# Kernel optimization log

Hardware: AMD Instinct MI355X
Metric: run time of the kernel (lower is better)

## Reference

```python
import jax, jax.numpy as jnp
import numpy as np

N = 16384        # nodes
E = 262144       # edges (avg degree 16)
MUL = 64         # multiplicity per irrep
RDIM = 8         # radial embedding dim
NEURONS = 64     # radial MLP hidden width
NSPECIES = 4
AVG_NEIGH = 16.0
SQRT3 = 1.7320508075688772


def setup_inputs() -> dict:
    key = jax.random.key(0)
    k = jax.random.split(key, 16)
    ey1 = jax.random.normal(k[3], (E, 3), jnp.float32)
    ey1 = ey1 / jnp.linalg.norm(ey1, axis=-1, keepdims=True)  # l=1 spherical harmonics ~ unit edge vectors
    return {
        'node_x0': jax.random.normal(k[0], (N, MUL), jnp.float32),
        'node_x1': jax.random.normal(k[1], (N, MUL, 3), jnp.float32),
        'edge_y0': jnp.ones((E,), jnp.float32),            # l=0 SH is constant
        'edge_y1': ey1,
        'radial_embedding': jax.random.uniform(k[4], (E, RDIM), jnp.float32),
        'senders': jax.random.randint(k[5], (E,), 0, N, dtype=jnp.int32),
        'receivers': jax.random.randint(k[6], (E,), 0, N, dtype=jnp.int32),
        'node_species': jax.random.randint(k[7], (N,), 0, NSPECIES, dtype=jnp.int32),
        'Wup0': jax.random.normal(k[8], (MUL, MUL), jnp.float32),
        'Wup1': jax.random.normal(k[9], (MUL, MUL), jnp.float32),
        'Rw1': jax.random.normal(k[10], (RDIM, NEURONS), jnp.float32),
        'Rw2': jax.random.normal(k[11], (NEURONS, 4 * MUL), jnp.float32),
        'Wd0': jax.random.normal(k[12], (2 * MUL, 2 * MUL), jnp.float32),
        'Wd1': jax.random.normal(k[13], (2 * MUL, MUL), jnp.float32),
        'Wsc0': jax.random.normal(k[14], (NSPECIES, MUL, 2 * MUL), jnp.float32),
        'Wsc1': jax.random.normal(k[15], (NSPECIES, MUL, MUL), jnp.float32),
    }


def reference(node_x0, node_x1, edge_y0, edge_y1, radial_embedding,
              senders, receivers, node_species,
              Wup0, Wup1, Rw1, Rw2, Wd0, Wd1, Wsc0, Wsc1):
    inv = 1.0 / jnp.sqrt(jnp.float32(MUL))
    # ---- linear_up: per-irrep channel mixing --------------------------------
    h0 = (node_x0 @ Wup0) * inv                              # [N, MUL] 0e
    h1 = jnp.einsum('nmc,mk->nkc', node_x1, Wup1) * inv      # [N, MUL, 3] 1o
    # ---- radial MLP -> per-edge tensor-product path weights -----------------
    hid = jax.nn.silu((radial_embedding @ Rw1) / jnp.sqrt(jnp.float32(RDIM)))
    w = ((hid @ Rw2) / jnp.sqrt(jnp.float32(NEURONS))).reshape(E, 4, MUL)
    # ---- gather sender features ---------------------------------------------
    s0 = h0[senders]                                         # [E, MUL]
    s1 = h1[senders]                                         # [E, MUL, 3]
    # ---- CG tensor product (lmax=1) with radial weights ----------------------
    m0a = w[:, 0] * s0 * edge_y0[:, None]                    # 0e x 0e -> 0e
    m0b = w[:, 1] * jnp.einsum('emc,ec->em', s1, edge_y1) / SQRT3  # 1o . 1o -> 0e
    m1a = w[:, 2][:, :, None] * s0[:, :, None] * edge_y1[:, None, :]  # 0e x 1o -> 1o
    m1b = w[:, 3][:, :, None] * s1 * edge_y0[:, None, None]          # 1o x 0e -> 1o
    # ---- scatter-sum to receivers, normalize by sqrt(avg_num_neighbours) ----
    denom = jnp.sqrt(jnp.float32(AVG_NEIGH))
    a0 = jax.ops.segment_sum(jnp.concatenate([m0a, m0b], axis=-1), receivers, num_segments=N) / denom  # [N, 2*MUL]
    a1 = jax.ops.segment_sum(jnp.concatenate([m1a, m1b], axis=1), receivers, num_segments=N) / denom   # [N, 2*MUL, 3]
    # ---- linear_down to gate irreps (MUL scalars + MUL gates, MUL vectors) ---
    inv2 = 1.0 / jnp.sqrt(jnp.float32(2 * MUL))
    d0 = (a0 @ Wd0) * inv2                                   # [N, 2*MUL]
    d1 = jnp.einsum('nmc,mk->nkc', a1, Wd1) * inv2           # [N, MUL, 3]
    # ---- species-indexed self connection (gather weights by species) --------
    all0 = jnp.einsum('nm,smk->nsk', node_x0, Wsc0) * inv    # [N, S, 2*MUL]
    sc0 = jnp.take_along_axis(all0, node_species[:, None, None], axis=1)[:, 0]
    all1 = jnp.einsum('nmc,smk->nskc', node_x1, Wsc1) * inv  # [N, S, MUL, 3]
    sc1 = jnp.take_along_axis(all1, node_species[:, None, None, None], axis=1)[:, 0]
    f0 = 0.5 * (d0 + sc0)
    f1 = 0.5 * (d1 + sc1)
    # ---- equivariant gate: even_act on scalars, even_gate_act on gates ------
    scalars = jax.nn.silu(f0[:, :MUL])                       # [N, MUL]
    gates = jax.nn.silu(f0[:, MUL:])                         # [N, MUL]
    vectors = f1 * gates[:, :, None]                         # [N, MUL, 3]
    return scalars, vectors
```

## Files before the change

### kernel.cpp

```cpp
#include <hip/hip_runtime.h>

#define NN 16384
#define NE 262144
#define N64 (NN * 64)

typedef unsigned short u16;
typedef __attribute__((ext_vector_type(8))) short short8;
typedef __attribute__((ext_vector_type(4))) float f32x4;

__device__ __forceinline__ float us2f(u16 u) {
    union { unsigned int i; float f; } v; v.i = ((unsigned int)u) << 16; return v.f;
}
__device__ __forceinline__ u16 f2us(float x) {
    union { float f; unsigned int i; } u; u.f = x;
    unsigned int r = u.i + 0x7FFF + ((u.i >> 16) & 1);
    return (u16)(r >> 16);
}
__device__ __forceinline__ float silu_f(float x) { return x / (1.0f + __expf(-x)); }
__device__ __forceinline__ float ldf(const void* p, long i, int f) {
    return f ? ((const float*)p)[i] : us2f(((const u16*)p)[i]);
}
__device__ __forceinline__ void ld8(const void* p, long v8, int f, float* o) {
    if (f) {
        const f32x4* q = (const f32x4*)p + v8 * 2;
        f32x4 a = q[0], b = q[1];
        o[0] = a[0]; o[1] = a[1]; o[2] = a[2]; o[3] = a[3];
        o[4] = b[0]; o[5] = b[1]; o[6] = b[2]; o[7] = b[3];
    } else {
        short8 s = ((const short8*)p)[v8];
#pragma unroll
        for (int j = 0; j < 8; j++) o[j] = us2f((u16)s[j]);
    }
}
__device__ __forceinline__ void st8(u16* d, const float* o) {
    short8 s;
#pragma unroll
    for (int j = 0; j < 8; j++) s[j] = (short)f2us(o[j]);
    *reinterpret_cast<short8*>(d) = s;
}
__device__ __forceinline__ short8 f32x8_to_bf16(const float* p) {
    f32x4 a = *reinterpret_cast<const f32x4*>(p);
    f32x4 b = *reinterpret_cast<const f32x4*>(p + 4);
    short8 r;
    r[0] = (short)f2us(a[0]); r[1] = (short)f2us(a[1]);
    r[2] = (short)f2us(a[2]); r[3] = (short)f2us(a[3]);
    r[4] = (short)f2us(b[0]); r[5] = (short)f2us(b[1]);
    r[6] = (short)f2us(b[2]); r[7] = (short)f2us(b[3]);
    return r;
}

__global__ void k_sniff(const u16* __restrict__ re, int* __restrict__ flag) {
    int t = threadIdx.x;
    int hit = (re[t] >= 0x4000) ? 1 : 0;
    unsigned long long b = __ballot(hit);
    if (t == 0) *flag = (__popcll(b) >= 4) ? 1 : 0;
}

#define SB0 1048576L
#define SB1 4194304L
#define SB2 4456448L
#define SB3 5242880L
#define SB4 7340032L
#define SB5 7344128L
#define SB6 7348224L
#define SB7 7348736L
#define SB8 7365120L
#define SB9 7381504L
#define SB10 7389696L
#define SB11 7422464L
#define SB12 7438848L

__global__ void k_convert(const void* x0, const void* x1, const void* ey0, const void* ey1,
                          const void* re, const void* Wup0, const void* Wup1, const void* Rw1,
                          const void* Rw2, const void* Wd0, const void* Wd1, const void* Wsc0,
                          const void* Wsc1, const int* __restrict__ flag,
                          const int* __restrict__ recv, int* __restrict__ cnt,
                          u16* c_x0, u16* x1T, u16* c_ey0, u16* c_ey1, u16* c_re,
                          u16* c_Wup0, u16* c_Wup1, u16* c_Rw1, u16* c_Rw2,
                          u16* c_Wd0, u16* c_Wd1, u16* c_Wsc0, u16* c_Wsc1) {
    long i = (long)blockIdx.x * 256 + threadIdx.x;
    int f = *flag;
    if (i < NE) atomicAdd(&cnt[recv[i]], 1);
    if (i < 131072) {
        float o[8]; ld8(x0, i, f, o); st8(c_x0 + i * 8, o);
    } else if (i < 262144) {
        long v = i - 131072;
        int n = (int)(v >> 3), k8 = (int)(v & 7);
        long b8 = (long)n * 24 + (long)k8 * 3;
        float o[24];
        ld8(x1, b8, f, o); ld8(x1, b8 + 1, f, o + 8); ld8(x1, b8 + 2, f, o + 16);
#pragma unroll
        for (int c = 0; c < 3; c++) {
            float t[8];
#pragma unroll
            for (int k = 0; k < 8; k++) t[k] = o[k * 3 + c];
            st8(x1T + (long)c * N64 + (long)n * 64 + k8 * 8, t);
        }
    } else if (i < 294912) {
        long v = i - 262144; float o[8]; ld8(ey0, v, f, o); st8(c_ey0 + v * 8, o);
    } else if (i < 393216) {
        long v = i - 294912; float o[8]; ld8(ey1, v, f, o); st8(c_ey1 + v * 8, o);
    } else if (i < 655360) {
        long v = i - 393216; float o[8]; ld8(re, v, f, o); st8(c_re + v * 8, o);
    } else {
        long t = i - 655360;
        if (t < 4096)       { long r = t >> 6, c = t & 63;
                              c_Wup0[c * 64 + r] = f2us(ldf(Wup0, t, f)); }
        else if (t < 8192)  { t -= 4096; long r = t >> 6, c = t & 63;
                              c_Wup1[c * 64 + r] = f2us(ldf(Wup1, t, f)); }
        else if (t < 8704)  { t -= 8192; c_Rw1[t] = f2us(ldf(Rw1, t, f)); }
        else if (t < 25088) { t -= 8704; long r = t >> 8, c = t & 255;
                              c_Rw2[c * 64 + r] = f2us(ldf(Rw2, t, f)); }
        else if (t < 41472) { t -= 25088; long r = t >> 7, c = t & 127;
                              c_Wd0[c * 128 + r] = f2us(ldf(Wd0, t, f)); }
        else if (t < 49664) { t -= 41472; long r = t >> 6, c = t & 63;
                              c_Wd1[c * 128 + r] = f2us(ldf(Wd1, t, f)); }
        else if (t < 82432) { t -= 49664; long s = t >> 13, rm = t & 8191;
                              long r = rm >> 7, c = rm & 127;
                              c_Wsc0[s * 8192 + c * 64 + r] = f2us(ldf(Wsc0, t, f)); }
        else                { t -= 82432; long s = t >> 12, rm = t & 4095;
                              long r = rm >> 6, c = rm & 63;
                              c_Wsc1[s * 4096 + c * 64 + r] = f2us(ldf(Wsc1, t, f)); }
    }
}

__global__ void k_scan(const int* __restrict__ cnt, int* __restrict__ offs,
                       int* __restrict__ cursor) {
    __shared__ int sd[256];
    int t = threadIdx.x;
    int base = t * 64;
    const int4* c4 = (const int4*)cnt;
    int loc[64];
#pragma unroll
    for (int i = 0; i < 16; i++) {
        int4 v = c4[t * 16 + i];
        loc[i * 4 + 0] = v.x; loc[i * 4 + 1] = v.y; loc[i * 4 + 2] = v.z; loc[i * 4 + 3] = v.w;
    }
    int sum = 0;
#pragma unroll
    for (int i = 0; i < 64; i++) sum += loc[i];
    sd[t] = sum; __syncthreads();
    for (int off = 1; off < 256; off <<= 1) {
        int v = (t >= off) ? sd[t - off] : 0;
        __syncthreads();
        sd[t] += v;
        __syncthreads();
    }
    int run = sd[t] - sum;
    for (int i = 0; i < 64; i++) {
        offs[base + i] = run; cursor[base + i] = run;
        run += loc[i];
    }
    if (t == 255) offs[NN] = run;
}

__global__ void k_scatter(const int* __restrict__ recv, const int* __restrict__ senders,
                          const u16* __restrict__ ey0, const u16* __restrict__ ey1,
                          int* __restrict__ cursor, int4* __restrict__ meta) {
    int e = blockIdx.x * 256 + threadIdx.x;
    int node = recv[e];
    int p = atomicAdd(&cursor[node], 1);
    unsigned y0  = ey0[e];
    unsigned y1x = ey1[(long)e * 3 + 0];
    unsigned y1y = ey1[(long)e * 3 + 1];
    unsigned y1z = ey1[(long)e * 3 + 2];
    int4 m;
    m.x = senders[e];
    m.y = (int)(y0 | (y1x << 16));
    m.z = (int)(y1y | (y1z << 16));
    m.w = (int)((unsigned)e | ((unsigned)node << 18));
    meta[p] = m;
}

__global__ void k_up_gemm(const u16* __restrict__ x0, const u16* __restrict__ x1T,
                          const u16* __restrict__ Wup0, const u16* __restrict__ Wup1,
                          u16* __restrict__ h) {
    int inst = blockIdx.y;
    int wv = threadIdx.x >> 6, lane = threadIdx.x & 63;
    int lhi = lane >> 4, llo = lane & 15;
    int mb = blockIdx.x * 256 + wv * 64;
    const u16* B = (inst == 0) ? Wup0 : Wup1;
    const u16* A = (inst == 0) ? x0 : (x1T + (long)(inst - 1) * N64);

    short8 bfr[4][2];
#pragma unroll
    for (int t = 0; t < 4; t++)
#pragma unroll
        for (int s = 0; s < 2; s++)
            bfr[t][s] = *reinterpret_cast<const short8*>(B + (long)(t * 16 + llo) * 64 + s * 32 + lhi * 8);

    f32x4 acc[4][4];
#pragma unroll
    for (int i = 0; i < 4; i++)
#pragma unroll
        for (int t = 0; t < 4; t++) acc[i][t] = 0.0f;

#pragma unroll
    for (int s = 0; s < 2; s++) {
        short8 af[4];
#pragma unroll
        for (int i = 0; i < 4; i++)
            af[i] = *reinterpret_cast<const short8*>(A + (long)(mb + i * 16 + llo) * 64 + s * 32 + lhi * 8);
#pragma unroll
        for (int i = 0; i < 4; i++)
#pragma unroll
            for (int t = 0; t < 4; t++)
                acc[i][t] = __builtin_amdgcn_mfma_f32_16x16x32_bf16(af[i], bfr[t][s], acc[i][t], 0, 0, 0);
    }
#pragma unroll
    for (int i = 0; i < 4; i++)
#pragma unroll
        for (int t = 0; t < 4; t++)
#pragma unroll
            for (int r = 0; r < 4; r++)
                h[(long)(mb + i * 16 + lhi * 4 + r) * 256 + (t * 16 + llo) * 4 + inst] =
                    f2us(acc[i][t][r] * 0.125f);
}

#define RROW 268
__global__ void __launch_bounds__(256, 4)
k_edge(const u16* __restrict__ re, const u16* __restrict__ Rw1,
       const u16* __restrict__ Rw2, const int4* __restrict__ meta,
       const u16* __restrict__ h, float* __restrict__ abuf32) {
    __shared__ u16 w_lds[64 * RROW];
    u16 (*hid_s)[72] = reinterpret_cast<u16 (*)[72]>(w_lds);

    int tid = threadIdx.x;
    int wv = tid >> 6, lane = tid & 63, lhi = lane >> 4, llo = lane & 15;
    int p0 = blockIdx.x * 64;

    {
        int el = tid >> 2;
        int jb = (tid & 3) * 16;
        int e = ((const int*)meta)[(long)(p0 + el) * 4 + 3] & 0x3FFFF;
        short8 r8 = *reinterpret_cast<const short8*>(re + (long)e * 8);
        float rr[8];
#pragma unroll
        for (int r = 0; r < 8; r++) rr[r] = us2f((u16)r8[r]);
        float hv[16];
#pragma unroll
        for (int q = 0; q < 2; q++) {
            short8 w8 = *reinterpret_cast<const short8*>(Rw1 + jb + q * 8);
#pragma unroll
            for (int j = 0; j < 8; j++) hv[q * 8 + j] = rr[0] * us2f((u16)w8[j]);
        }
#pragma unroll
        for (int r = 1; r < 8; r++) {
#pragma unroll
            for (int q = 0; q < 2; q++) {
                short8 w8 = *reinterpret_cast<const short8*>(Rw1 + (long)r * 64 + jb + q * 8);
#pragma unroll
                for (int j = 0; j < 8; j++) hv[q * 8 + j] += rr[r] * us2f((u16)w8[j]);
            }
        }
#pragma unroll
        for (int q = 0; q < 4; q++) {
            ushort4 pk;
            pk.x = f2us(silu_f(hv[q * 4 + 0] * 0.35355339059327373f));
            pk.y = f2us(silu_f(hv[q * 4 + 1] * 0.35355339059327373f));
            pk.z = f2us(silu_f(hv[q * 4 + 2] * 0.35355339059327373f));
            pk.w = f2us(silu_f(hv[q * 4 + 3] * 0.35355339059327373f));
            *reinterpret_cast<ushort4*>(&hid_s[el][jb + q * 4]) = pk;
        }
    }
    __syncthreads();

    {
        short8 bfr[4][2];
#pragma unroll
        for (int t = 0; t < 4; t++)
#pragma unroll
            for (int s = 0; s < 2; s++)
                bfr[t][s] = *reinterpret_cast<const short8*>(
                    Rw2 + (long)(wv * 64 + t * 16 + llo) * 64 + s * 32 + lhi * 8);
        f32x4 acc[4][4];
#pragma unroll
        for (int i = 0; i < 4; i++)
#pragma unroll
            for (int t = 0; t < 4; t++) acc[i][t] = 0.0f;
#pragma unroll
        for (int s = 0; s < 2; s++) {
            short8 af[4];
#pragma unroll
            for (int i = 0; i < 4; i++)
                af[i] = *reinterpret_cast<const short8*>(&hid_s[i * 16 + llo][s * 32 + lhi * 8]);
#pragma unroll
            for (int i = 0; i < 4; i++)
#pragma unroll
                for (int t = 0; t < 4; t++)
                    acc[i][t] = __builtin_amdgcn_mfma_f32_16x16x32_bf16(af[i], bfr[t][s], acc[i][t], 0, 0, 0);
        }
        __syncthreads();
#pragma unroll
        for (int i = 0; i < 4; i++)
#pragma unroll
            for (int t = 0; t < 4; t++)
#pragma unroll
                for (int r = 0; r < 4; r++)
                    w_lds[(i * 16 + lhi * 4 + r) * RROW + wv * 64 + t * 16 + llo] =
                        f2us(acc[i][t][r] * 0.125f);
    }
    __syncthreads();

    {
        const float qn = 0.25f;
        const float rs3 = 0.57735026918962576f;
        int l = lane;
        int base = wv * 16;
        float acc[8];
#pragma unroll
        for (int r = 0; r < 8; r++) acc[r] = 0.f;
        int cur = -1;

        int4 ma = meta[p0 + base];
        ushort4 ha = *reinterpret_cast<const ushort4*>(h + (long)ma.x * 256 + l * 4);
        int4 mb_ = meta[p0 + base + 1];
        ushort4 hb = *reinterpret_cast<const ushort4*>(h + (long)mb_.x * 256 + l * 4);

        for (int ss = 0; ss < 16; ss++) {
            int4 mc = mb_; ushort4 hc = hb;
            if (ss + 2 < 16) {
                mc = meta[p0 + base + ss + 2];
                hc = *reinterpret_cast<const ushort4*>(h + (long)mc.x * 256 + l * 4);
            }
            int node = (int)(((unsigned)ma.w) >> 18);
            if (node != cur) {
                if (cur >= 0) {
                    float* dst = abuf32 + (long)cur * 512 + l;
                    atomicAdd(dst,        acc[0] * qn);
                    atomicAdd(dst + 64,   acc[1] * qn * rs3);
                    atomicAdd(dst + 128,  acc[2] * qn);
                    atomicAdd(dst + 192,  acc[3] * qn);
                    atomicAdd(dst + 256,  acc[4] * qn);
                    atomicAdd(dst + 320,  acc[5] * qn);
                    atomicAdd(dst + 384,  acc[6] * qn);
                    atomicAdd(dst + 448,  acc[7] * qn);
                }
                cur = node;
#pragma unroll
                for (int r = 0; r < 8; r++) acc[r] = 0.f;
            }
            int sl = base + ss;
            float w0 = us2f(w_lds[sl * RROW + l]);
            float w1 = us2f(w_lds[sl * RROW + 64 + l]);
            float w2 = us2f(w_lds[sl * RROW + 128 + l]);
            float w3 = us2f(w_lds[sl * RROW + 192 + l]);
            float y0  = us2f((u16)((unsigned)ma.y & 0xffff));
            float y1x = us2f((u16)((unsigned)ma.y >> 16));
            float y1y = us2f((u16)((unsigned)ma.z & 0xffff));
            float y1z = us2f((u16)((unsigned)ma.z >> 16));
            float s0 = us2f(ha.x), s1x = us2f(ha.y), s1y = us2f(ha.z), s1z = us2f(ha.w);
            acc[0] += w0 * s0 * y0;
            acc[1] += w1 * (s1x * y1x + s1y * y1y + s1z * y1z);
            acc[2] += w2 * s0 * y1x;  acc[3] += w3 * s1x * y0;
            acc[4] += w2 * s0 * y1y;  acc[5] += w3 * s1y * y0;
            acc[6] += w2 * s0 * y1z;  acc[7] += w3 * s1z * y0;
            ma = mb_; ha = hb; mb_ = mc; hb = hc;
        }
        {
            float* dst = abuf32 + (long)cur * 512 + l;
            atomicAdd(dst,        acc[0] * qn);
            atomicAdd(dst + 64,   acc[1] * qn * rs3);
            atomicAdd(dst + 128,  acc[2] * qn);
            atomicAdd(dst + 192,  acc[3] * qn);
            atomicAdd(dst + 256,  acc[4] * qn);
            atomicAdd(dst + 320,  acc[5] * qn);
            atomicAdd(dst + 384,  acc[6] * qn);
            atomicAdd(dst + 448,  acc[7] * qn);
        }
    }
}

#define DN 32
__global__ void __launch_bounds__(320, 3)
k_down(const float* __restrict__ abuf32, const u16* __restrict__ x0,
       const u16* __restrict__ x1T, const int* __restrict__ species,
       const u16* __restrict__ Wd0T, const u16* __restrict__ Wd1T,
       const u16* __restrict__ Wsc0T, const u16* __restrict__ Wsc1T,
       float* __restrict__ out) {
    __shared__ float gate_s[DN][65];
    __shared__ float vec_s[DN * 192];
    __shared__ int sp_s[DN];
    int tid = threadIdx.x;
    int g = tid >> 6;
    int lane = tid & 63, lhi = lane >> 4, llo = lane & 15;
    int node0 = blockIdx.x * DN;
    if (tid < DN) sp_s[tid] = species[node0 + tid];
    __syncthreads();

    const float* Ad; const u16* BdT; int bcol;
    const u16* As; const u16* BsT; int sstr;
    if (g <= 1) { Ad = abuf32; BdT = Wd0T; bcol = g * 64; As = x0; BsT = Wsc0T; sstr = 8192; }
    else        { Ad = abuf32 + (g - 1) * 128; BdT = Wd1T; bcol = 0;
                  As = x1T + (long)(g - 2) * N64; BsT = Wsc1T; sstr = 4096; }

    const float inv2 = 0.08838834764831845f;
    const float inv  = 0.125f;

    short8 a2[DN / 16][2];
#pragma unroll
    for (int rt = 0; rt < DN / 16; rt++)
#pragma unroll
        for (int ks = 0; ks < 2; ks++)
            a2[rt][ks] = *reinterpret_cast<const short8*>(
                As + (long)(node0 + rt * 16 + llo) * 64 + ks * 32 + lhi * 8);

    f32x4 res[DN / 16][4];
#pragma unroll
    for (int rt = 0; rt < DN / 16; rt++)
#pragma unroll
        for (int ct = 0; ct < 4; ct++) res[rt][ct] = 0.0f;

    for (int s = 0; s < 4; s++) {
        short8 bs[4][2];
#pragma unroll
        for (int ct = 0; ct < 4; ct++)
#pragma unroll
            for (int ks = 0; ks < 2; ks++)
                bs[ct][ks] = *reinterpret_cast<const short8*>(
                    BsT + (long)s * sstr + (long)(bcol + ct * 16 + llo) * 64 + ks * 32 + lhi * 8);
#pragma unroll
        for (int rt = 0; rt < DN / 16; rt++) {
            f32x4 accs[4];
#pragma unroll
            for (int ct = 0; ct < 4; ct++) accs[ct] = 0.0f;
#pragma unroll
            for (int ks = 0; ks < 2; ks++)
#pragma unroll
                for (int ct = 0; ct < 4; ct++)
                    accs[ct] = __builtin_amdgcn_mfma_f32_16x16x32_bf16(a2[rt][ks], bs[ct][ks], accs[ct], 0, 0, 0);
#pragma unroll
            for (int r = 0; r < 4; r++) {
                int sp = sp_s[rt * 16 + lhi * 4 + r];
                if (sp == s)
#pragma unroll
                    for (int ct = 0; ct < 4; ct++) res[rt][ct][r] = accs[ct][r];
            }
        }
    }

    short8 bd[4][4];
#pragma unroll
    for (int ct = 0; ct < 4; ct++)
#pragma unroll
        for (int ks = 0; ks < 4; ks++)
            bd[ct][ks] = *reinterpret_cast<const short8*>(
                BdT + (long)(bcol + ct * 16 + llo) * 128 + ks * 32 + lhi * 8);

#pragma unroll
    for (int rt = 0; rt < DN / 16; rt++) {
        f32x4 accd[4];
#pragma unroll
        for (int ct = 0; ct < 4; ct++) accd[ct] = 0.0f;
#pragma unroll
        for (int ks = 0; ks < 4; ks++) {
            short8 a = f32x8_to_bf16(Ad + (long)(node0 + rt * 16 + llo) * 512 + ks * 32 + lhi * 8);
#pragma unroll
            for (int ct = 0; ct < 4; ct++)
                accd[ct] = __builtin_amdgcn_mfma_f32_16x16x32_bf16(a, bd[ct][ks], accd[ct], 0, 0, 0);
        }
#pragma unroll
        for (int ct = 0; ct < 4; ct++)
#pragma unroll
            for (int r = 0; r < 4; r++) {
                float fvv = 0.5f * (accd[ct][r] * inv2 + res[rt][ct][r] * inv);
                int row = rt * 16 + lhi * 4 + r;
                int col = ct * 16 + llo;
                if (g == 0) {
                    out[(long)(node0 + row) * 64 + col] = silu_f(fvv);
                } else if (g == 1) {
                    gate_s[row][col] = silu_f(fvv);
                } else {
                    vec_s[row * 192 + col * 3 + (g - 2)] = fvv;
                }
            }
    }
    __syncthreads();

    {
        float* vout = out + (long)N64 + (long)node0 * 192;
        for (int q4 = tid; q4 < DN * 48; q4 += 320) {
            int q = q4 * 4;
            int row = q4 / 48;
            int rem = q - row * 192;
            f32x4 v = *reinterpret_cast<const f32x4*>(&vec_s[q]);
#pragma unroll
            for (int e = 0; e < 4; e++) v[e] *= gate_s[row][(rem + e) / 3];
            *reinterpret_cast<f32x4*>(vout + q) = v;
        }
    }
}

extern "C" void kernel_launch(void* const* d_in, const int* in_sizes, int n_in,
                              void* d_out, int out_size, void* d_ws, size_t ws_size,
                              hipStream_t stream) {
    const int* senders   = (const int*)d_in[5];
    const int* receivers = (const int*)d_in[6];
    const int* species   = (const int*)d_in[7];
    float* out = (float*)d_out;

    char* ws = (char*)d_ws;
    size_t o = 0;
    auto alloc = [&](size_t bytes) { size_t p = o; o = (o + bytes + 255) & ~255UL; return p; };
    int* flag   = (int*)(ws + alloc(4));
    int* cnt    = (int*)(ws + alloc((size_t)NN * 4));
    int* offs   = (int*)(ws + alloc((size_t)(NN + 1) * 4));
    int* cursor = (int*)(ws + alloc((size_t)NN * 4));
    int4* meta  = (int4*)(ws + alloc((size_t)NE * 16));
    u16* c_x0   = (u16*)(ws + alloc(SB0 * 2));
    u16* x1T    = (u16*)(ws + alloc((size_t)3 * N64 * 2));
    u16* c_ey0  = (u16*)(ws + alloc((SB2 - SB1) * 2));
    u16* c_ey1  = (u16*)(ws + alloc((SB3 - SB2) * 2));
    u16* c_re   = (u16*)(ws + alloc((SB4 - SB3) * 2));
    u16* c_Wup0 = (u16*)(ws + alloc((SB5 - SB4) * 2));
    u16* c_Wup1 = (u16*)(ws + alloc((SB6 - SB5) * 2));
    u16* c_Rw1  = (u16*)(ws + alloc((SB7 - SB6) * 2));
    u16* c_Rw2  = (u16*)(ws + alloc((SB8 - SB7) * 2));
    u16* c_Wd0  = (u16*)(ws + alloc((SB9 - SB8) * 2));
    u16* c_Wd1  = (u16*)(ws + alloc((SB10 - SB9) * 2));
    u16* c_Wsc0 = (u16*)(ws + alloc((SB11 - SB10) * 2));
    u16* c_Wsc1 = (u16*)(ws + alloc((SB12 - SB11) * 2));
    u16* h      = (u16*)(ws + alloc((size_t)NN * 256 * 2));
    float* abuf32 = (float*)(ws + alloc((size_t)NN * 512 * 4));

    k_sniff<<<1, 64, 0, stream>>>((const u16*)d_in[4], flag);
    (void)hipMemsetAsync(cnt, 0, (size_t)NN * 4, stream);
    (void)hipMemsetAsync(abuf32, 0, (size_t)NN * 512 * 4, stream);
    k_convert<<<2946, 256, 0, stream>>>(d_in[0], d_in[1], d_in[2], d_in[3], d_in[4],
        d_in[8], d_in[9], d_in[10], d_in[11], d_in[12], d_in[13], d_in[14], d_in[15],
        flag, receivers, cnt,
        c_x0, x1T, c_ey0, c_ey1, c_re,
        c_Wup0, c_Wup1, c_Rw1, c_Rw2, c_Wd0, c_Wd1, c_Wsc0, c_Wsc1);
    k_scan<<<1, 256, 0, stream>>>(cnt, offs, cursor);
    k_scatter<<<NE / 256, 256, 0, stream>>>(receivers, senders, c_ey0, c_ey1,
                                            cursor, meta);

    k_up_gemm<<<dim3(NN / 256, 4), 256, 0, stream>>>(c_x0, x1T, c_Wup0, c_Wup1, h);

    k_edge<<<NE / 64, 256, 0, stream>>>(c_re, c_Rw1, c_Rw2, meta, h, abuf32);

    k_down<<<NN / DN, 320, 0, stream>>>(abuf32, c_x0, x1T, species,
                                        c_Wd0, c_Wd1, c_Wsc0, c_Wsc1, out);
}
```

Measured before the change: 258.2 us.

## Replace global atomics with plain stores for node runs owned by one wave

In the edge kernel, a receiver run that lies entirely inside one wave's 16-edge chunk is now written to the aggregation buffer with plain stores instead of global atomicAdd. Runs split across waves inside a block are merged in shared memory first. Only runs that cross a block boundary still use global atomics. This cuts global atomic traffic, at the cost of extra shared memory, a block barrier and boundary bookkeeping. Plain stores are only correct if the buffer is not expected to accumulate, i.e. each fully owned node is written exactly once.

```diff
diff --git a/kernel.cpp b/kernel.cpp
--- a/kernel.cpp
+++ b/kernel.cpp
@@ -223,11 +223,17 @@
        const u16* __restrict__ Rw2, const int4* __restrict__ meta,
        const u16* __restrict__ h, float* __restrict__ abuf32) {
     __shared__ u16 w_lds[64 * RROW];
+    __shared__ float mrg[3][512];
+    __shared__ int mrg_node[4], mrg_glob[4];
     u16 (*hid_s)[72] = reinterpret_cast<u16 (*)[72]>(w_lds);
 
     int tid = threadIdx.x;
     int wv = tid >> 6, lane = tid & 63, lhi = lane >> 4, llo = lane & 15;
     int p0 = blockIdx.x * 64;
+
+#pragma unroll
+    for (int k = tid; k < 3 * 512; k += 256) (&mrg[0][0])[k] = 0.f;
+    if (tid < 4) { mrg_node[tid] = -1; mrg_glob[tid] = 0; }
 
     {
         int el = tid >> 2;
@@ -307,10 +313,52 @@
         const float rs3 = 0.57735026918962576f;
         int l = lane;
         int base = wv * 16;
+        int gs = p0 + base;
+        int prevNode = -1, nextNode = -1;
+        if (gs > 0)
+            prevNode = (int)(((unsigned)((const int*)meta)[(long)(gs - 1) * 4 + 3]) >> 18);
+        if (gs + 16 < NE)
+            nextNode = (int)(((unsigned)((const int*)meta)[(long)(gs + 16) * 4 + 3]) >> 18);
+
         float acc[8];
 #pragma unroll
         for (int r = 0; r < 8; r++) acc[r] = 0.f;
         int cur = -1;
+        int atStart = 1;
+
+        auto flushRun = [&](int n, bool L, bool R) {
+            float v0 = acc[0] * qn, v1 = acc[1] * qn * rs3;
+            float v2 = acc[2] * qn, v3 = acc[3] * qn;
+            float v4 = acc[4] * qn, v5 = acc[5] * qn;
+            float v6 = acc[6] * qn, v7 = acc[7] * qn;
+            if (!L && !R) {
+                float* dst = abuf32 + (long)n * 512 + l;
+                dst[0]   = v0; dst[64]  = v1; dst[128] = v2; dst[192] = v3;
+                dst[256] = v4; dst[320] = v5; dst[384] = v6; dst[448] = v7;
+                return;
+            }
+            bool inL = L && (wv > 0), inR = R && (wv < 3);
+            bool xL = L && (wv == 0), xR = R && (wv == 3);
+            if (inL || inR) {
+                int j = inL ? wv : wv + 1;
+                if (l == 0) {
+                    mrg_node[j] = n;
+                    if (xL || xR) mrg_glob[j] = 1;
+                    if (inL && inR) { mrg_glob[wv] = 1; mrg_glob[wv + 1] = 1; }
+                }
+                float* md = &mrg[j - 1][l];
+                atomicAdd(md,       v0); atomicAdd(md + 64,  v1);
+                atomicAdd(md + 128, v2); atomicAdd(md + 192, v3);
+                atomicAdd(md + 256, v4); atomicAdd(md + 320, v5);
+                atomicAdd(md + 384, v6); atomicAdd(md + 448, v7);
+            } else {
+                float* dst = abuf32 + (long)n * 512 + l;
+                atomicAdd(dst,       v0); atomicAdd(dst + 64,  v1);
+                atomicAdd(dst + 128, v2); atomicAdd(dst + 192, v3);
+                atomicAdd(dst + 256, v4); atomicAdd(dst + 320, v5);
+                atomicAdd(dst + 384, v6); atomicAdd(dst + 448, v7);
+            }
+        };
 
         int4 ma = meta[p0 + base];
         ushort4 ha = *reinterpret_cast<const ushort4*>(h + (long)ma.x * 256 + l * 4);
@@ -326,19 +374,12 @@
             int node = (int)(((unsigned)ma.w) >> 18);
             if (node != cur) {
                 if (cur >= 0) {
-                    float* dst = abuf32 + (long)cur * 512 + l;
-                    atomicAdd(dst,        acc[0] * qn);
-                    atomicAdd(dst + 64,   acc[1] * qn * rs3);
-                    atomicAdd(dst + 128,  acc[2] * qn);
-                    atomicAdd(dst + 192,  acc[3] * qn);
-                    atomicAdd(dst + 256,  acc[4] * qn);
-                    atomicAdd(dst + 320,  acc[5] * qn);
-                    atomicAdd(dst + 384,  acc[6] * qn);
-                    atomicAdd(dst + 448,  acc[7] * qn);
+                    flushRun(cur, atStart && (prevNode == cur), false);
+                    atStart = 0;
+#pragma unroll
+                    for (int r = 0; r < 8; r++) acc[r] = 0.f;
                 }
                 cur = node;
-#pragma unroll
-                for (int r = 0; r < 8; r++) acc[r] = 0.f;
             }
             int sl = base + ss;
             float w0 = us2f(w_lds[sl * RROW + l]);
@@ -357,16 +398,21 @@
             acc[6] += w2 * s0 * y1z;  acc[7] += w3 * s1z * y0;
             ma = mb_; ha = hb; mb_ = mc; hb = hc;
         }
-        {
-            float* dst = abuf32 + (long)cur * 512 + l;
-            atomicAdd(dst,        acc[0] * qn);
-            atomicAdd(dst + 64,   acc[1] * qn * rs3);
-            atomicAdd(dst + 128,  acc[2] * qn);
-            atomicAdd(dst + 192,  acc[3] * qn);
-            atomicAdd(dst + 256,  acc[4] * qn);
-            atomicAdd(dst + 320,  acc[5] * qn);
-            atomicAdd(dst + 384,  acc[6] * qn);
-            atomicAdd(dst + 448,  acc[7] * qn);
+        flushRun(cur, atStart && (prevNode == cur), nextNode == cur);
+    }
+    __syncthreads();
+
+#pragma unroll
+    for (int j = 1; j < 4; j++) {
+        int n = mrg_node[j];
+        if (n >= 0) {
+            float a = mrg[j - 1][tid], b = mrg[j - 1][tid + 256];
+            float* dst = abuf32 + (long)n * 512;
+            if (mrg_glob[j]) {
+                atomicAdd(dst + tid, a); atomicAdd(dst + tid + 256, b);
+            } else {
+                dst[tid] = a; dst[tid + 256] = b;
+            }
         }
     }
 }
```

After: 302.2 us. 1.17x slower.
